# Kernel optimization log

Measured on AMD Instinct MI355X. Metric: run time of the kernel, lower is better.

The kernel has to match this reference:

```python
import jax, jax.numpy as jnp
import numpy as np

B = 8192; N = 50; NUM_NODES = 200000; NUM_EDGES = 1000000
FEAT = 64; EFEAT = 4; TD = 16; D = 64


def setup_inputs() -> dict:
    key = jax.random.key(0)
    ks = jax.random.split(key, 32)
    p = lambda i, shape: jax.random.normal(ks[i], shape, jnp.float32) * 0.05
    inp = {}
    nf = jax.random.normal(ks[0], (NUM_NODES, FEAT), jnp.float32)
    skills = jax.random.randint(ks[1], (NUM_NODES,), 0, 100).astype(jnp.float32)
    inp['node_raw_features'] = nf.at[:, 0].set(skills)  # col 0 = skill id
    inp['edge_raw_features'] = jax.random.normal(ks[2], (NUM_EDGES, EFEAT), jnp.float32)
    inp['src_node_ids'] = jax.random.randint(ks[3], (B,), 0, NUM_NODES)
    inp['dst_node_ids'] = jax.random.randint(ks[4], (B,), 0, NUM_NODES)
    inp['node_interact_times'] = jax.random.uniform(ks[5], (B,), jnp.float32, 0.0, 1e4)
    inp['src_neighbor_node_ids'] = jax.random.randint(ks[6], (B, N), 0, NUM_NODES)
    inp['src_neighbor_edge_ids'] = jax.random.randint(ks[7], (B, N), 0, NUM_EDGES)
    inp['src_neighbor_times'] = jax.random.uniform(ks[8], (B, N), jnp.float32, 0.0, 1e4)
    inp['dst_neighbor_node_ids'] = jax.random.randint(ks[9], (B, N), 0, NUM_NODES)
    inp['dst_neighbor_edge_ids'] = jax.random.randint(ks[10], (B, N), 0, NUM_EDGES)
    inp['dst_neighbor_times'] = jax.random.uniform(ks[11], (B, N), jnp.float32, 0.0, 1e4)
    # projection layers
    inp['W_feat'] = p(12, (FEAT, D)); inp['b_feat'] = p(13, (D,))
    inp['W_edge'] = p(14, (1, D));    inp['b_edge'] = p(15, (D,))
    inp['W_time'] = p(16, (TD, D));   inp['b_time'] = p(17, (D,))
    inp['W_struct'] = p(18, (1, D));  inp['b_struct'] = p(19, (D,))
    inp['W_out'] = p(20, (D, D));     inp['b_out'] = p(21, (D,))
    # time encoder (cos(w*dt + b), trainable Linear(1, TD) as in TGN TimeEncoder)
    inp['time_w'] = p(22, (TD,)); inp['time_b'] = p(23, (TD,))
    # src / dst GRUs (PyTorch layout: W_ih [3H,E], W_hh [3H,H])
    inp['src_W_ih'] = p(24, (3 * D, D)); inp['src_W_hh'] = p(25, (3 * D, D))
    inp['src_b_ih'] = p(26, (3 * D,));   inp['src_b_hh'] = p(27, (3 * D,))
    inp['dst_W_ih'] = p(28, (3 * D, D)); inp['dst_W_hh'] = p(29, (3 * D, D))
    inp['dst_b_ih'] = p(30, (3 * D,));   inp['dst_b_hh'] = p(31, (3 * D,))
    return inp


def _lin(x, W, b):
    return x @ W + b


def _gru_last_hidden(x, W_ih, W_hh, b_ih, b_hh):
    # x: [B, T, E] -> final hidden state [B, H] (PyTorch GRU equations)
    Bb, _, _ = x.shape
    H = W_hh.shape[1]

    def step(h, xt):
        gi = xt @ W_ih.T + b_ih            # [B, 3H]
        gh = h @ W_hh.T + b_hh             # [B, 3H]
        ir, iz, inn = jnp.split(gi, 3, axis=-1)
        hr, hz, hn = jnp.split(gh, 3, axis=-1)
        r = jax.nn.sigmoid(ir + hr)
        z = jax.nn.sigmoid(iz + hz)
        n = jnp.tanh(inn + r * hn)
        h_new = (1.0 - z) * n + z * h
        return h_new, None

    h0 = jnp.zeros((Bb, H), x.dtype)
    hT, _ = jax.lax.scan(step, h0, jnp.swapaxes(x, 0, 1))
    return hT


def reference(node_raw_features, edge_raw_features, src_node_ids, dst_node_ids,
              node_interact_times, src_neighbor_node_ids, src_neighbor_edge_ids,
              src_neighbor_times, dst_neighbor_node_ids, dst_neighbor_edge_ids,
              dst_neighbor_times, W_feat, b_feat, W_edge, b_edge, W_time, b_time,
              W_struct, b_struct, W_out, b_out, time_w, time_b,
              src_W_ih, src_W_hh, src_b_ih, src_b_hh,
              dst_W_ih, dst_W_hh, dst_b_ih, dst_b_hh):
    t = node_interact_times
    # append the query interaction itself (edge id 0) -> [B, N+1]
    src_nids = jnp.concatenate([src_neighbor_node_ids, src_node_ids[:, None]], 1)
    src_eids = jnp.concatenate([src_neighbor_edge_ids, jnp.zeros_like(src_node_ids)[:, None]], 1)
    src_ts = jnp.concatenate([src_neighbor_times, t[:, None]], 1)
    dst_nids = jnp.concatenate([dst_neighbor_node_ids, dst_node_ids[:, None]], 1)
    dst_eids = jnp.concatenate([dst_neighbor_edge_ids, jnp.zeros_like(dst_node_ids)[:, None]], 1)
    dst_ts = jnp.concatenate([dst_neighbor_times, t[:, None]], 1)

    # co-occurrence features [B, N, 1]
    co_src = (src_neighbor_node_ids == dst_node_ids[:, None]).astype(jnp.float32)[..., None]
    co_dst = (dst_neighbor_node_ids == src_node_ids[:, None]).astype(jnp.float32)[..., None]
    # skill match features [B, N, 1]
    src_skill = node_raw_features[src_nids][:, :-1, 0].astype(jnp.int32)
    dst_skill = node_raw_features[dst_nids][:, -1, 0].astype(jnp.int32)[:, None]
    skill_f = (src_skill == dst_skill).astype(jnp.float32)[..., None]

    src_struct = _lin(co_src, W_struct, b_struct)
    dst_struct = _lin(co_dst, W_struct, b_struct)
    skill_struct = _lin(skill_f, W_struct, b_struct)

    def get_feats(nids, eids, ts):
        node_f = _lin(node_raw_features[nids], W_feat, b_feat)        # [B,N+1,D]
        delta = t[:, None] - ts                                       # dual-decay ablation: delta times
        tenc = jnp.cos(delta[..., None] * time_w + time_b)            # [B,N+1,TD]
        time_f = _lin(tenc, W_time, b_time)                           # [B,N+1,D]
        edge_f = _lin(edge_raw_features[eids][..., :1], W_edge, b_edge)
        return node_f, edge_f, time_f

    sn, se, st = get_feats(src_nids, src_eids, src_ts)
    dn, de, dt = get_feats(dst_nids, dst_eids, dst_ts)
    src_feats = sn + se + st
    dst_feats = dn + de + dt

    src_emb = _gru_last_hidden(src_feats[:, :-1] + skill_struct + src_struct,
                               src_W_ih, src_W_hh, src_b_ih, src_b_hh) + (se + st)[:, -1]
    dst_emb = _gru_last_hidden((de + dt)[:, :-1] + dst_struct,
                               dst_W_ih, dst_W_hh, dst_b_ih, dst_b_hh) + dst_feats[:, -1]

    return _lin(src_emb, W_out, b_out), _lin(dst_emb, W_out, b_out)
```

## Files before the change

### kernel.cpp

```cpp
#include <hip/hip_runtime.h>
#include <stdint.h>

#define BB 8192
#define NN 50

typedef _Float16 half8 __attribute__((ext_vector_type(8)));
typedef float floatx4 __attribute__((ext_vector_type(4)));

union FragU { uint4 u; half8 h; };
static __device__ __forceinline__ half8 u2h(uint4 u) { FragU f; f.u = u; return f.h; }

static __device__ __forceinline__ uint32_t pk2u(float a, float b) {
    auto p = __builtin_amdgcn_cvt_pkrtz(a, b);
    uint32_t u; __builtin_memcpy(&u, &p, 4); return u;
}

#define MFMA(A, B, C) __builtin_amdgcn_mfma_f32_16x16x32_f16((A), (B), (C), 0, 0, 0)

static __device__ __forceinline__ float frcp(float x) {
#if __has_builtin(__builtin_amdgcn_rcpf)
    return __builtin_amdgcn_rcpf(x);
#else
    return 1.0f / x;
#endif
}
static __device__ __forceinline__ float fexp2(float x) {
#if __has_builtin(__builtin_amdgcn_exp2f)
    return __builtin_amdgcn_exp2f(x);
#else
    return __expf(0.69314718056f * x);
#endif
}
static __device__ __forceinline__ float fsig(float x)   { return frcp(1.0f + fexp2(-1.44269504089f * x)); }
static __device__ __forceinline__ float ftanhf(float x) { return 1.0f - 2.0f * frcp(fexp2(2.88539008178f * x) + 1.0f); }

static __device__ __forceinline__ void bar_lds() {
    asm volatile("s_waitcnt lgkmcnt(0)" ::: "memory");
    __builtin_amdgcn_s_barrier();
}

__global__ __launch_bounds__(128, 2)
void dygkt4(const float* __restrict__ nodef, const float* __restrict__ edgef,
            const int* __restrict__ src_ids, const int* __restrict__ dst_ids,
            const float* __restrict__ times,
            const int* __restrict__ s_nids, const int* __restrict__ s_eids,
            const float* __restrict__ s_ts,
            const int* __restrict__ d_nids, const int* __restrict__ d_eids,
            const float* __restrict__ d_ts,
            const float* __restrict__ W_feat, const float* __restrict__ b_feat,
            const float* __restrict__ W_edge, const float* __restrict__ b_edge,
            const float* __restrict__ W_time, const float* __restrict__ b_time,
            const float* __restrict__ W_str,  const float* __restrict__ b_str,
            const float* __restrict__ W_out,  const float* __restrict__ b_out,
            const float* __restrict__ time_w, const float* __restrict__ time_b,
            const float* __restrict__ sWih, const float* __restrict__ sWhh,
            const float* __restrict__ sbih, const float* __restrict__ sbhh,
            const float* __restrict__ dWih, const float* __restrict__ dWhh,
            const float* __restrict__ dbih, const float* __restrict__ dbhh,
            float* __restrict__ out)
{
    __shared__ uint4 wfA[8][64];
    __shared__ uint4 woA[8][64];
    __shared__ __align__(16) _Float16 xls[2][16 * 72];
    __shared__ __align__(16) _Float16 hls[2][16 * 72];

    const int tid = threadIdx.x, w = tid >> 6, lane = tid & 63;
    const int g = lane >> 4, i16 = lane & 15;
    const bool is_src = blockIdx.x < 512;
    const int ib0 = (int)(blockIdx.x & 511) * 16;
    const int b = ib0 + i16;

    for (int q = tid; q < 512; q += 128) {
        int l = q & 63, tt = q >> 6;
        int kh = tt >> 2, mt = tt & 3, gg = l >> 4, ii = l & 15;
        float v[8], u[8];
        #pragma unroll
        for (int j = 0; j < 8; ++j) {
            int k = 32 * kh + 8 * gg + j, m = 16 * mt + ii;
            v[j] = W_feat[k * 64 + m];
            u[j] = W_out[k * 64 + m];
        }
        wfA[tt][l] = make_uint4(pk2u(v[0],v[1]), pk2u(v[2],v[3]), pk2u(v[4],v[5]), pk2u(v[6],v[7]));
        woA[tt][l] = make_uint4(pk2u(u[0],u[1]), pk2u(u[2],u[3]), pk2u(u[4],u[5]), pk2u(u[6],u[7]));
    }
    for (int q = tid; q < 16 * 72 / 2; q += 128) ((uint32_t*)hls[0])[q] = 0u;
    __syncthreads();

    const float* WI = is_src ? sWih : dWih;
    const float* WH = is_src ? sWhh : dWhh;
    uint4 wih[6][2], whh[6][2];
    #pragma unroll
    for (int gt = 0; gt < 3; ++gt)
        #pragma unroll
        for (int tq = 0; tq < 2; ++tq)
            #pragma unroll
            for (int kh = 0; kh < 2; ++kh) {
                int row = 64 * gt + 16 * (2 * w + tq) + i16;
                const float* p = WI + (size_t)row * 64 + 32 * kh + 8 * g;
                float4 a = *(const float4*)p, c = *(const float4*)(p + 4);
                wih[gt * 2 + tq][kh] = make_uint4(pk2u(a.x,a.y), pk2u(a.z,a.w), pk2u(c.x,c.y), pk2u(c.z,c.w));
                const float* qq = WH + (size_t)row * 64 + 32 * kh + 8 * g;
                float4 e = *(const float4*)qq, f = *(const float4*)(qq + 4);
                whh[gt * 2 + tq][kh] = make_uint4(pk2u(e.x,e.y), pk2u(e.z,e.w), pk2u(f.x,f.y), pk2u(f.z,f.w));
            }

    uint4 wtA[2];
    #pragma unroll
    for (int tq = 0; tq < 2; ++tq) {
        int mt = 2 * w + tq;
        float v[8];
        #pragma unroll
        for (int j = 0; j < 8; ++j) {
            int k = 8 * g + j, dim = 16 * mt + i16;
            float x = 0.0f;
            if (k < 16)       x = W_time[k * 64 + dim];
            else if (k == 16) x = W_edge[dim];
            else if (k == 17) x = W_str[dim];
            else if (k == 18) x = b_edge[dim] + b_time[dim];
            else if (k == 19) x = is_src ? (b_feat[dim] + 2.0f * b_str[dim]) : b_str[dim];
            else if (k == 20) x = b_feat[dim];
            v[j] = x;
        }
        wtA[tq] = make_uint4(pk2u(v[0],v[1]), pk2u(v[2],v[3]), pk2u(v[4],v[5]), pk2u(v[6],v[7]));
    }

    const float* BI = is_src ? sbih : dbih;
    const float* BH = is_src ? sbhh : dbhh;
    floatx4 brz[4], bin[2], bhn[2];
    #pragma unroll
    for (int gz = 0; gz < 2; ++gz)
        #pragma unroll
        for (int tq = 0; tq < 2; ++tq) {
            int r0 = 64 * gz + 16 * (2 * w + tq) + 4 * g;
            floatx4 v;
            #pragma unroll
            for (int r = 0; r < 4; ++r) v[r] = BI[r0 + r] + BH[r0 + r];
            brz[gz * 2 + tq] = v;
        }
    #pragma unroll
    for (int tq = 0; tq < 2; ++tq) {
        int r0 = 128 + 16 * (2 * w + tq) + 4 * g;
        floatx4 vi, vh;
        #pragma unroll
        for (int r = 0; r < 4; ++r) { vi[r] = BI[r0 + r]; vh[r] = BH[r0 + r]; }
        bin[tq] = vi; bhn[tq] = vh;
    }

    const int* pn = (is_src ? s_nids : d_nids) + (size_t)b * NN;
    const int* pe = (is_src ? s_eids : d_eids) + (size_t)b * NN;
    const float* pt = (is_src ? s_ts : d_ts) + (size_t)b * NN;
    const float tqL = times[b];
    const int didL = dst_ids[b];
    const int oid = is_src ? didL : src_ids[b];
    const float dskill = is_src ? nodef[(size_t)didL * 64] : 0.0f;
    float twc[8], tbc[8];
    #pragma unroll
    for (int j = 0; j < 8; ++j) {
        int k = 8 * (g & 1) + j;
        twc[j] = time_w[k]; tbc[j] = time_b[k];
    }

    int nidC = pn[0], eidC = pe[0];
    float tsC = pt[0];
    float e0C = edgef[4 * (size_t)eidC];
    float4 nfa = {0,0,0,0}, nfb = {0,0,0,0}, nfc = {0,0,0,0}, nfd = {0,0,0,0};
    if (is_src) {
        const float* rp = nodef + (size_t)nidC * 64 + 8 * g;
        nfa = *(const float4*)rp;        nfb = *(const float4*)(rp + 4);
        nfc = *(const float4*)(rp + 32); nfd = *(const float4*)(rp + 36);
    }

    floatx4 hM[2] = {{0,0,0,0},{0,0,0,0}};
    const floatx4 z4 = {0,0,0,0};
    int cur = 0;

    for (int t = 0; t < NN; ++t) {
        int nidN = 0, eidN = 0; float tsN = 0.0f;
        if (t + 1 < NN) { nidN = pn[t + 1]; eidN = pe[t + 1]; tsN = pt[t + 1]; }

        float nsk = __shfl(nfa.x, i16);
        float sf = ((nidC == oid) ? 1.0f : 0.0f) +
                   ((is_src && nsk == dskill) ? 1.0f : 0.0f);
        float delta = tqL - tsC;
        uint4 tb4;
        if (g < 2) {
            float cv[8];
            #pragma unroll
            for (int j = 0; j < 8; ++j) cv[j] = __cosf(delta * twc[j] + tbc[j]);
            tb4 = make_uint4(pk2u(cv[0],cv[1]), pk2u(cv[2],cv[3]), pk2u(cv[4],cv[5]), pk2u(cv[6],cv[7]));
        } else if (g == 2) {
            tb4 = make_uint4(pk2u(e0C, sf), pk2u(1.0f, 1.0f), 0u, 0u);
        } else {
            tb4 = make_uint4(0u, 0u, 0u, 0u);
        }
        half8 tB = u2h(tb4);

        floatx4 xacc[2];
        if (is_src) {
            uint4 nf0 = make_uint4(pk2u(nfa.x,nfa.y), pk2u(nfa.z,nfa.w), pk2u(nfb.x,nfb.y), pk2u(nfb.z,nfb.w));
            uint4 nf1 = make_uint4(pk2u(nfc.x,nfc.y), pk2u(nfc.z,nfc.w), pk2u(nfd.x,nfd.y), pk2u(nfd.z,nfd.w));
            half8 nB0 = u2h(nf0), nB1 = u2h(nf1);
            #pragma unroll
            for (int tq = 0; tq < 2; ++tq) {
                int mt = 2 * w + tq;
                floatx4 a = MFMA(u2h(wfA[mt][lane]), nB0, z4);
                a = MFMA(u2h(wfA[4 + mt][lane]), nB1, a);
                xacc[tq] = MFMA(u2h(wtA[tq]), tB, a);
            }
        } else {
            #pragma unroll
            for (int tq = 0; tq < 2; ++tq) xacc[tq] = MFMA(u2h(wtA[tq]), tB, z4);
        }

        #pragma unroll
        for (int tq = 0; tq < 2; ++tq)
            *(uint2*)&xls[cur][i16 * 72 + 32 * w + 16 * tq + 4 * g] =
                make_uint2(pk2u(xacc[tq][0], xacc[tq][1]), pk2u(xacc[tq][2], xacc[tq][3]));

        float e0N = 0.0f; float4 na = {0,0,0,0}, nb = {0,0,0,0}, nc = {0,0,0,0}, nd = {0,0,0,0};
        if (t + 1 < NN) {
            e0N = edgef[4 * (size_t)eidN];
            if (is_src) {
                const float* rp = nodef + (size_t)nidN * 64 + 8 * g;
                na = *(const float4*)rp;        nb = *(const float4*)(rp + 4);
                nc = *(const float4*)(rp + 32); nd = *(const float4*)(rp + 36);
            }
        }

        bar_lds();

        half8 xB0 = u2h(*(const uint4*)&xls[cur][i16 * 72 + 8 * g]);
        half8 xB1 = u2h(*(const uint4*)&xls[cur][i16 * 72 + 32 + 8 * g]);
        half8 hB0 = u2h(*(const uint4*)&hls[cur][i16 * 72 + 8 * g]);
        half8 hB1 = u2h(*(const uint4*)&hls[cur][i16 * 72 + 32 + 8 * g]);

        floatx4 rg[2], zg[2], ia[2], ha[2];
        #pragma unroll
        for (int tq = 0; tq < 2; ++tq) {
            floatx4 a = MFMA(u2h(wih[tq][0]), xB0, brz[tq]);
            a = MFMA(u2h(wih[tq][1]), xB1, a);
            a = MFMA(u2h(whh[tq][0]), hB0, a);
            rg[tq] = MFMA(u2h(whh[tq][1]), hB1, a);
        }
        #pragma unroll
        for (int tq = 0; tq < 2; ++tq) {
            floatx4 a = MFMA(u2h(wih[2 + tq][0]), xB0, brz[2 + tq]);
            a = MFMA(u2h(wih[2 + tq][1]), xB1, a);
            a = MFMA(u2h(whh[2 + tq][0]), hB0, a);
            zg[tq] = MFMA(u2h(whh[2 + tq][1]), hB1, a);
        }
        #pragma unroll
        for (int tq = 0; tq < 2; ++tq) {
            floatx4 a = MFMA(u2h(wih[4 + tq][0]), xB0, bin[tq]);
            ia[tq] = MFMA(u2h(wih[4 + tq][1]), xB1, a);
            floatx4 c = MFMA(u2h(whh[4 + tq][0]), hB0, bhn[tq]);
            ha[tq] = MFMA(u2h(whh[4 + tq][1]), hB1, c);
        }

        #pragma unroll
        for (int tq = 0; tq < 2; ++tq)
            #pragma unroll
            for (int r = 0; r < 4; ++r) {
                float rr = fsig(rg[tq][r]);
                float zz = fsig(zg[tq][r]);
                float nn = ftanhf(ia[tq][r] + rr * ha[tq][r]);
                hM[tq][r] = nn + zz * (hM[tq][r] - nn);
            }

        #pragma unroll
        for (int tq = 0; tq < 2; ++tq)
            *(uint2*)&hls[cur ^ 1][i16 * 72 + 32 * w + 16 * tq + 4 * g] =
                make_uint2(pk2u(hM[tq][0], hM[tq][1]), pk2u(hM[tq][2], hM[tq][3]));

        cur ^= 1;
        nidC = nidN; eidC = eidN; tsC = tsN; e0C = e0N;
        nfa = na; nfb = nb; nfc = nc; nfd = nd;
    }

    float e00 = edgef[0];
    uint4 tt4;
    if (g < 2) {
        float cv[8];
        #pragma unroll
        for (int j = 0; j < 8; ++j) cv[j] = __cosf(tbc[j]);
        tt4 = make_uint4(pk2u(cv[0],cv[1]), pk2u(cv[2],cv[3]), pk2u(cv[4],cv[5]), pk2u(cv[6],cv[7]));
    } else if (g == 2) {
        tt4 = make_uint4(pk2u(e00, 0.0f), pk2u(1.0f, 0.0f), pk2u(is_src ? 0.0f : 1.0f, 0.0f), 0u);
    } else {
        tt4 = make_uint4(0u, 0u, 0u, 0u);
    }
    half8 tT = u2h(tt4);

    floatx4 tacc[2];
    #pragma unroll
    for (int tq = 0; tq < 2; ++tq) tacc[tq] = MFMA(u2h(wtA[tq]), tT, z4);
    if (!is_src) {
        const float* rp = nodef + (size_t)didL * 64 + 8 * g;
        float4 da = *(const float4*)rp,        db = *(const float4*)(rp + 4);
        float4 dc = *(const float4*)(rp + 32), dd = *(const float4*)(rp + 36);
        uint4 d0 = make_uint4(pk2u(da.x,da.y), pk2u(da.z,da.w), pk2u(db.x,db.y), pk2u(db.z,db.w));
        uint4 d1 = make_uint4(pk2u(dc.x,dc.y), pk2u(dc.z,dc.w), pk2u(dd.x,dd.y), pk2u(dd.z,dd.w));
        #pragma unroll
        for (int tq = 0; tq < 2; ++tq) {
            int mt = 2 * w + tq;
            tacc[tq] = MFMA(u2h(wfA[mt][lane]), u2h(d0), tacc[tq]);
            tacc[tq] = MFMA(u2h(wfA[4 + mt][lane]), u2h(d1), tacc[tq]);
        }
    }

    #pragma unroll
    for (int tq = 0; tq < 2; ++tq) {
        floatx4 e = hM[tq] + tacc[tq];
        *(uint2*)&xls[0][i16 * 72 + 32 * w + 16 * tq + 4 * g] =
            make_uint2(pk2u(e[0], e[1]), pk2u(e[2], e[3]));
    }
    bar_lds();
    half8 eB0 = u2h(*(const uint4*)&xls[0][i16 * 72 + 8 * g]);
    half8 eB1 = u2h(*(const uint4*)&xls[0][i16 * 72 + 32 + 8 * g]);

    const size_t obase = (is_src ? 0 : (size_t)BB * 64) + (size_t)b * 64;
    #pragma unroll
    for (int tq = 0; tq < 2; ++tq) {
        int mt = 2 * w + tq;
        floatx4 bo;
        #pragma unroll
        for (int r = 0; r < 4; ++r) bo[r] = b_out[16 * mt + 4 * g + r];
        floatx4 o = MFMA(u2h(woA[mt][lane]), eB0, bo);
        o = MFMA(u2h(woA[4 + mt][lane]), eB1, o);
        *(floatx4*)(out + obase + 16 * mt + 4 * g) = o;
    }
}

extern "C" void kernel_launch(void* const* d_in, const int* in_sizes, int n_in,
                              void* d_out, int out_size, void* d_ws, size_t ws_size,
                              hipStream_t stream) {
    (void)in_sizes; (void)n_in; (void)d_ws; (void)ws_size; (void)out_size;
    const float* nodef  = (const float*)d_in[0];
    const float* edgef  = (const float*)d_in[1];
    const int*   srcid  = (const int*)  d_in[2];
    const int*   dstid  = (const int*)  d_in[3];
    const float* times  = (const float*)d_in[4];
    const int*   s_nids = (const int*)  d_in[5];
    const int*   s_eids = (const int*)  d_in[6];
    const float* s_ts   = (const float*)d_in[7];
    const int*   d_nids = (const int*)  d_in[8];
    const int*   d_eids = (const int*)  d_in[9];
    const float* d_ts   = (const float*)d_in[10];
    const float* W_feat = (const float*)d_in[11];
    const float* b_feat = (const float*)d_in[12];
    const float* W_edge = (const float*)d_in[13];
    const float* b_edge = (const float*)d_in[14];
    const float* W_time = (const float*)d_in[15];
    const float* b_time = (const float*)d_in[16];
    const float* W_str  = (const float*)d_in[17];
    const float* b_str  = (const float*)d_in[18];
    const float* W_out  = (const float*)d_in[19];
    const float* b_out  = (const float*)d_in[20];
    const float* time_w = (const float*)d_in[21];
    const float* time_b = (const float*)d_in[22];
    const float* sWih   = (const float*)d_in[23];
    const float* sWhh   = (const float*)d_in[24];
    const float* sbih   = (const float*)d_in[25];
    const float* sbhh   = (const float*)d_in[26];
    const float* dWih   = (const float*)d_in[27];
    const float* dWhh   = (const float*)d_in[28];
    const float* dbih   = (const float*)d_in[29];
    const float* dbhh   = (const float*)d_in[30];

    dim3 grid(1024), block(128);
    dygkt4<<<grid, block, 0, stream>>>(
        nodef, edgef, srcid, dstid, times,
        s_nids, s_eids, s_ts, d_nids, d_eids, d_ts,
        W_feat, b_feat, W_edge, b_edge, W_time, b_time,
        W_str, b_str, W_out, b_out, time_w, time_b,
        sWih, sWhh, sbih, sbhh, dWih, dWhh, dbih, dbhh,
        (float*)d_out);
}
```

Measured before the change: 245.5 us.

## Prefold gate scale constants into GRU weights and software-pipeline time encoding

Folds the sigmoid/tanh exp2 scale factors into the fp16 GRU weights and biases, which removes per-element multiplies in the recurrent gate math. Computes the next step's cosine time encoding and skill flag after the hidden MFMAs so that transcendental work overlaps with the recurrence. Also interleaves src/dst blocks by blockIdx parity, moves the first barrier later, and replaces the vector output store with scalar stores. Scaling in fp16 before conversion may change rounding slightly.

```diff
diff --git a/kernel.cpp b/kernel.cpp
--- a/kernel.cpp
+++ b/kernel.cpp
@@ -31,8 +31,6 @@
     return __expf(0.69314718056f * x);
 #endif
 }
-static __device__ __forceinline__ float fsig(float x)   { return frcp(1.0f + fexp2(-1.44269504089f * x)); }
-static __device__ __forceinline__ float ftanhf(float x) { return 1.0f - 2.0f * frcp(fexp2(2.88539008178f * x) + 1.0f); }
 
 static __device__ __forceinline__ void bar_lds() {
     asm volatile("s_waitcnt lgkmcnt(0)" ::: "memory");
@@ -40,24 +38,24 @@
 }
 
 __global__ __launch_bounds__(128, 2)
-void dygkt4(const float* __restrict__ nodef, const float* __restrict__ edgef,
-            const int* __restrict__ src_ids, const int* __restrict__ dst_ids,
-            const float* __restrict__ times,
-            const int* __restrict__ s_nids, const int* __restrict__ s_eids,
-            const float* __restrict__ s_ts,
-            const int* __restrict__ d_nids, const int* __restrict__ d_eids,
-            const float* __restrict__ d_ts,
-            const float* __restrict__ W_feat, const float* __restrict__ b_feat,
-            const float* __restrict__ W_edge, const float* __restrict__ b_edge,
-            const float* __restrict__ W_time, const float* __restrict__ b_time,
-            const float* __restrict__ W_str,  const float* __restrict__ b_str,
-            const float* __restrict__ W_out,  const float* __restrict__ b_out,
-            const float* __restrict__ time_w, const float* __restrict__ time_b,
-            const float* __restrict__ sWih, const float* __restrict__ sWhh,
-            const float* __restrict__ sbih, const float* __restrict__ sbhh,
-            const float* __restrict__ dWih, const float* __restrict__ dWhh,
-            const float* __restrict__ dbih, const float* __restrict__ dbhh,
-            float* __restrict__ out)
+void dygkt10(const float* __restrict__ nodef, const float* __restrict__ edgef,
+             const int* __restrict__ src_ids, const int* __restrict__ dst_ids,
+             const float* __restrict__ times,
+             const int* __restrict__ s_nids, const int* __restrict__ s_eids,
+             const float* __restrict__ s_ts,
+             const int* __restrict__ d_nids, const int* __restrict__ d_eids,
+             const float* __restrict__ d_ts,
+             const float* __restrict__ W_feat, const float* __restrict__ b_feat,
+             const float* __restrict__ W_edge, const float* __restrict__ b_edge,
+             const float* __restrict__ W_time, const float* __restrict__ b_time,
+             const float* __restrict__ W_str,  const float* __restrict__ b_str,
+             const float* __restrict__ W_out,  const float* __restrict__ b_out,
+             const float* __restrict__ time_w, const float* __restrict__ time_b,
+             const float* __restrict__ sWih, const float* __restrict__ sWhh,
+             const float* __restrict__ sbih, const float* __restrict__ sbhh,
+             const float* __restrict__ dWih, const float* __restrict__ dWhh,
+             const float* __restrict__ dbih, const float* __restrict__ dbhh,
+             float* __restrict__ out)
 {
     __shared__ uint4 wfA[8][64];
     __shared__ uint4 woA[8][64];
@@ -66,9 +64,12 @@
 
     const int tid = threadIdx.x, w = tid >> 6, lane = tid & 63;
     const int g = lane >> 4, i16 = lane & 15;
-    const bool is_src = blockIdx.x < 512;
-    const int ib0 = (int)(blockIdx.x & 511) * 16;
-    const int b = ib0 + i16;
+    const bool is_src = (blockIdx.x & 1) == 0;
+    const int b = (int)(blockIdx.x >> 1) * 16 + i16;
+
+    const float SRZ = -1.44269504089f;
+    const float SN  =  2.88539008178f;
+    const floatx4 z4 = {0, 0, 0, 0};
 
     for (int q = tid; q < 512; q += 128) {
         int l = q & 63, tt = q >> 6;
@@ -84,13 +85,13 @@
         woA[tt][l] = make_uint4(pk2u(u[0],u[1]), pk2u(u[2],u[3]), pk2u(u[4],u[5]), pk2u(u[6],u[7]));
     }
     for (int q = tid; q < 16 * 72 / 2; q += 128) ((uint32_t*)hls[0])[q] = 0u;
-    __syncthreads();
 
     const float* WI = is_src ? sWih : dWih;
     const float* WH = is_src ? sWhh : dWhh;
     uint4 wih[6][2], whh[6][2];
     #pragma unroll
-    for (int gt = 0; gt < 3; ++gt)
+    for (int gt = 0; gt < 3; ++gt) {
+        const float s = (gt == 2) ? SN : SRZ;
         #pragma unroll
         for (int tq = 0; tq < 2; ++tq)
             #pragma unroll
@@ -98,11 +99,14 @@
                 int row = 64 * gt + 16 * (2 * w + tq) + i16;
                 const float* p = WI + (size_t)row * 64 + 32 * kh + 8 * g;
                 float4 a = *(const float4*)p, c = *(const float4*)(p + 4);
-                wih[gt * 2 + tq][kh] = make_uint4(pk2u(a.x,a.y), pk2u(a.z,a.w), pk2u(c.x,c.y), pk2u(c.z,c.w));
+                wih[gt * 2 + tq][kh] = make_uint4(pk2u(s*a.x,s*a.y), pk2u(s*a.z,s*a.w),
+                                                  pk2u(s*c.x,s*c.y), pk2u(s*c.z,s*c.w));
                 const float* qq = WH + (size_t)row * 64 + 32 * kh + 8 * g;
                 float4 e = *(const float4*)qq, f = *(const float4*)(qq + 4);
-                whh[gt * 2 + tq][kh] = make_uint4(pk2u(e.x,e.y), pk2u(e.z,e.w), pk2u(f.x,f.y), pk2u(f.z,f.w));
+                whh[gt * 2 + tq][kh] = make_uint4(pk2u(s*e.x,s*e.y), pk2u(s*e.z,s*e.w),
+                                                  pk2u(s*f.x,s*f.y), pk2u(s*f.z,s*f.w));
             }
+    }
 
     uint4 wtA[2];
     #pragma unroll
@@ -134,7 +138,7 @@
             int r0 = 64 * gz + 16 * (2 * w + tq) + 4 * g;
             floatx4 v;
             #pragma unroll
-            for (int r = 0; r < 4; ++r) v[r] = BI[r0 + r] + BH[r0 + r];
+            for (int r = 0; r < 4; ++r) v[r] = SRZ * (BI[r0 + r] + BH[r0 + r]);
             brz[gz * 2 + tq] = v;
         }
     #pragma unroll
@@ -142,7 +146,7 @@
         int r0 = 128 + 16 * (2 * w + tq) + 4 * g;
         floatx4 vi, vh;
         #pragma unroll
-        for (int r = 0; r < 4; ++r) { vi[r] = BI[r0 + r]; vh[r] = BH[r0 + r]; }
+        for (int r = 0; r < 4; ++r) { vi[r] = SN * BI[r0 + r]; vh[r] = SN * BH[r0 + r]; }
         bin[tq] = vi; bhn[tq] = vh;
     }
 
@@ -160,70 +164,78 @@
         twc[j] = time_w[k]; tbc[j] = time_b[k];
     }
 
-    int nidC = pn[0], eidC = pe[0];
-    float tsC = pt[0];
-    float e0C = edgef[4 * (size_t)eidC];
+    __syncthreads();
+
     float4 nfa = {0,0,0,0}, nfb = {0,0,0,0}, nfc = {0,0,0,0}, nfd = {0,0,0,0};
-    if (is_src) {
-        const float* rp = nodef + (size_t)nidC * 64 + 8 * g;
-        nfa = *(const float4*)rp;        nfb = *(const float4*)(rp + 4);
-        nfc = *(const float4*)(rp + 32); nfd = *(const float4*)(rp + 36);
-    }
-
-    floatx4 hM[2] = {{0,0,0,0},{0,0,0,0}};
-    const floatx4 z4 = {0,0,0,0};
-    int cur = 0;
-
-    for (int t = 0; t < NN; ++t) {
-        int nidN = 0, eidN = 0; float tsN = 0.0f;
-        if (t + 1 < NN) { nidN = pn[t + 1]; eidN = pe[t + 1]; tsN = pt[t + 1]; }
-
-        float nsk = __shfl(nfa.x, i16);
-        float sf = ((nidC == oid) ? 1.0f : 0.0f) +
-                   ((is_src && nsk == dskill) ? 1.0f : 0.0f);
-        float delta = tqL - tsC;
-        uint4 tb4;
+    uint4 tb4C;
+    {
+        int nid0 = pn[0], eid0 = pe[0];
+        float ts0 = pt[0];
+        float e00v = edgef[4 * (size_t)eid0];
+        float nsk0 = 0.0f;
+        if (is_src) {
+            const float* rp = nodef + (size_t)nid0 * 64 + 8 * g;
+            nfa = *(const float4*)rp;        nfb = *(const float4*)(rp + 4);
+            nfc = *(const float4*)(rp + 32); nfd = *(const float4*)(rp + 36);
+            nsk0 = nodef[(size_t)nid0 * 64];
+        }
+        float sf = ((nid0 == oid) ? 1.0f : 0.0f) +
+                   ((is_src && nsk0 == dskill) ? 1.0f : 0.0f);
+        float delta = tqL - ts0;
         if (g < 2) {
             float cv[8];
             #pragma unroll
             for (int j = 0; j < 8; ++j) cv[j] = __cosf(delta * twc[j] + tbc[j]);
-            tb4 = make_uint4(pk2u(cv[0],cv[1]), pk2u(cv[2],cv[3]), pk2u(cv[4],cv[5]), pk2u(cv[6],cv[7]));
+            tb4C = make_uint4(pk2u(cv[0],cv[1]), pk2u(cv[2],cv[3]), pk2u(cv[4],cv[5]), pk2u(cv[6],cv[7]));
         } else if (g == 2) {
-            tb4 = make_uint4(pk2u(e0C, sf), pk2u(1.0f, 1.0f), 0u, 0u);
+            tb4C = make_uint4(pk2u(e00v, sf), pk2u(1.0f, 1.0f), 0u, 0u);
         } else {
-            tb4 = make_uint4(0u, 0u, 0u, 0u);
-        }
-        half8 tB = u2h(tb4);
-
-        floatx4 xacc[2];
-        if (is_src) {
-            uint4 nf0 = make_uint4(pk2u(nfa.x,nfa.y), pk2u(nfa.z,nfa.w), pk2u(nfb.x,nfb.y), pk2u(nfb.z,nfb.w));
-            uint4 nf1 = make_uint4(pk2u(nfc.x,nfc.y), pk2u(nfc.z,nfc.w), pk2u(nfd.x,nfd.y), pk2u(nfd.z,nfd.w));
-            half8 nB0 = u2h(nf0), nB1 = u2h(nf1);
-            #pragma unroll
-            for (int tq = 0; tq < 2; ++tq) {
-                int mt = 2 * w + tq;
-                floatx4 a = MFMA(u2h(wfA[mt][lane]), nB0, z4);
-                a = MFMA(u2h(wfA[4 + mt][lane]), nB1, a);
-                xacc[tq] = MFMA(u2h(wtA[tq]), tB, a);
+            tb4C = make_uint4(0u, 0u, 0u, 0u);
+        }
+    }
+
+    floatx4 hM[2] = {z4, z4};
+    int cur = 0;
+
+    for (int t = 0; t < NN; ++t) {
+        const bool hasn = (t + 1 < NN);
+        int nidN = 0, eidN = 0; float tsN = 0.0f;
+        if (hasn) { nidN = pn[t + 1]; eidN = pe[t + 1]; tsN = pt[t + 1]; }
+
+        {
+            half8 tB = u2h(tb4C);
+            if (is_src) {
+                uint4 nf0 = make_uint4(pk2u(nfa.x,nfa.y), pk2u(nfa.z,nfa.w), pk2u(nfb.x,nfb.y), pk2u(nfb.z,nfb.w));
+                uint4 nf1 = make_uint4(pk2u(nfc.x,nfc.y), pk2u(nfc.z,nfc.w), pk2u(nfd.x,nfd.y), pk2u(nfd.z,nfd.w));
+                half8 nB0 = u2h(nf0), nB1 = u2h(nf1);
+                #pragma unroll
+                for (int tq = 0; tq < 2; ++tq) {
+                    int mt = 2 * w + tq;
+                    floatx4 a = MFMA(u2h(wfA[mt][lane]), nB0, z4);
+                    a = MFMA(u2h(wfA[4 + mt][lane]), nB1, a);
+                    floatx4 xacc = MFMA(u2h(wtA[tq]), tB, a);
+                    *(uint2*)&xls[cur][i16 * 72 + 32 * w + 16 * tq + 4 * g] =
+                        make_uint2(pk2u(xacc[0], xacc[1]), pk2u(xacc[2], xacc[3]));
+                }
+            } else {
+                #pragma unroll
+                for (int tq = 0; tq < 2; ++tq) {
+                    floatx4 xacc = MFMA(u2h(wtA[tq]), tB, z4);
+                    *(uint2*)&xls[cur][i16 * 72 + 32 * w + 16 * tq + 4 * g] =
+                        make_uint2(pk2u(xacc[0], xacc[1]), pk2u(xacc[2], xacc[3]));
+                }
             }
-        } else {
-            #pragma unroll
-            for (int tq = 0; tq < 2; ++tq) xacc[tq] = MFMA(u2h(wtA[tq]), tB, z4);
-        }
-
-        #pragma unroll
-        for (int tq = 0; tq < 2; ++tq)
-            *(uint2*)&xls[cur][i16 * 72 + 32 * w + 16 * tq + 4 * g] =
-                make_uint2(pk2u(xacc[tq][0], xacc[tq][1]), pk2u(xacc[tq][2], xacc[tq][3]));
-
-        float e0N = 0.0f; float4 na = {0,0,0,0}, nb = {0,0,0,0}, nc = {0,0,0,0}, nd = {0,0,0,0};
-        if (t + 1 < NN) {
+        }
+
+        float e0N = 0.0f, nskN = 0.0f;
+        float4 na = {0,0,0,0}, nb = {0,0,0,0}, nc = {0,0,0,0}, nd = {0,0,0,0};
+        if (hasn) {
             e0N = edgef[4 * (size_t)eidN];
             if (is_src) {
                 const float* rp = nodef + (size_t)nidN * 64 + 8 * g;
                 na = *(const float4*)rp;        nb = *(const float4*)(rp + 4);
                 nc = *(const float4*)(rp + 32); nd = *(const float4*)(rp + 36);
+                nskN = nodef[(size_t)nidN * 64];
             }
         }
 
@@ -257,13 +269,29 @@
             ha[tq] = MFMA(u2h(whh[4 + tq][1]), hB1, c);
         }
 
+        uint4 tb4N = make_uint4(0u, 0u, 0u, 0u);
+        if (hasn) {
+            float sf = ((nidN == oid) ? 1.0f : 0.0f) +
+                       ((is_src && nskN == dskill) ? 1.0f : 0.0f);
+            float delta = tqL - tsN;
+            if (g < 2) {
+                float cv[8];
+                #pragma unroll
+                for (int j = 0; j < 8; ++j) cv[j] = __cosf(delta * twc[j] + tbc[j]);
+                tb4N = make_uint4(pk2u(cv[0],cv[1]), pk2u(cv[2],cv[3]), pk2u(cv[4],cv[5]), pk2u(cv[6],cv[7]));
+            } else if (g == 2) {
+                tb4N = make_uint4(pk2u(e0N, sf), pk2u(1.0f, 1.0f), 0u, 0u);
+            }
+        }
+
         #pragma unroll
         for (int tq = 0; tq < 2; ++tq)
             #pragma unroll
             for (int r = 0; r < 4; ++r) {
-                float rr = fsig(rg[tq][r]);
-                float zz = fsig(zg[tq][r]);
-                float nn = ftanhf(ia[tq][r] + rr * ha[tq][r]);
+                float rr = frcp(1.0f + fexp2(rg[tq][r]));
+                float zz = frcp(1.0f + fexp2(zg[tq][r]));
+                float vv = ia[tq][r] + rr * ha[tq][r];
+                float nn = 1.0f - 2.0f * frcp(fexp2(vv) + 1.0f);
                 hM[tq][r] = nn + zz * (hM[tq][r] - nn);
             }
 
@@ -272,9 +300,9 @@
             *(uint2*)&hls[cur ^ 1][i16 * 72 + 32 * w + 16 * tq + 4 * g] =
                 make_uint2(pk2u(hM[tq][0], hM[tq][1]), pk2u(hM[tq][2], hM[tq][3]));
 
+        tb4C = tb4N;
+        nfa = na; nfb = nb; nfc = nc; nfd = nd;
         cur ^= 1;
-        nidC = nidN; eidC = eidN; tsC = tsN; e0C = e0N;
-        nfa = na; nfb = nb; nfc = nc; nfd = nd;
     }
 
     float e00 = edgef[0];
@@ -327,7 +355,9 @@
         for (int r = 0; r < 4; ++r) bo[r] = b_out[16 * mt + 4 * g + r];
         floatx4 o = MFMA(u2h(woA[mt][lane]), eB0, bo);
         o = MFMA(u2h(woA[4 + mt][lane]), eB1, o);
-        *(floatx4*)(out + obase + 16 * mt + 4 * g) = o;
+        #pragma unroll
+        for (int r = 0; r < 4; ++r)
+            out[obase + 16 * mt + 4 * g + r] = o[r];
     }
 }
 
@@ -368,7 +398,7 @@
     const float* dbhh   = (const float*)d_in[30];
 
     dim3 grid(1024), block(128);
-    dygkt4<<<grid, block, 0, stream>>>(
+    dygkt10<<<grid, block, 0, stream>>>(
         nodef, edgef, srcid, dstid, times,
         s_nids, s_eids, s_ts, d_nids, d_eids, d_ts,
         W_feat, b_feat, W_edge, b_edge, W_time, b_time,
```

Result: slower. 270.0 us (+10.0%).
